# Kernel optimization log

Hardware: AMD Instinct MI355X
Metric: run time of the kernel (lower is better)

Reference implementation:

```python
import jax, jax.numpy as jnp
import numpy as np

B, S, H = 2, 2048, 3072
NH, NKV, HD = 24, 8, 128  # num_heads, num_kv_heads, head_dim


def setup_inputs() -> dict:
    key = jax.random.key(0)
    ks = jax.random.split(key, 5)
    scale = 0.02
    return {
        "hidden_states": jax.random.normal(ks[0], (B, S, H), dtype=jnp.float32),
        "attention_mask": jnp.zeros((B, 1, S, S), dtype=jnp.float32),
        "Wq": jax.random.normal(ks[1], (H, NH * HD), dtype=jnp.float32) * scale,
        "Wk": jax.random.normal(ks[2], (H, NKV * HD), dtype=jnp.float32) * scale,
        "Wv": jax.random.normal(ks[3], (H, NKV * HD), dtype=jnp.float32) * scale,
        "Wo": jax.random.normal(ks[4], (NH * HD, H), dtype=jnp.float32) * scale,
    }


def reference(hidden_states, attention_mask, Wq, Wk, Wv, Wo):
    b, s, _ = hidden_states.shape
    n_rep = NH // NKV
    # projections
    q = (hidden_states @ Wq).reshape(b, s, NH, HD).transpose(0, 2, 1, 3)   # [B,NH,S,D]
    k = (hidden_states @ Wk).reshape(b, s, NKV, HD).transpose(0, 2, 1, 3)  # [B,NKV,S,D]
    v = (hidden_states @ Wv).reshape(b, s, NKV, HD).transpose(0, 2, 1, 3)
    # grouped-query attention: view q as [B, NKV, n_rep, S, D]; avoids materializing repeated KV
    qg = q.reshape(b, NKV, n_rep, s, HD)
    scores = jnp.einsum("bgrqd,bgkd->bgrqk", qg, k) / jnp.sqrt(jnp.float32(HD))
    scores = scores.reshape(b, NH, s, s) + attention_mask
    attn = jax.nn.softmax(scores.astype(jnp.float32), axis=-1).astype(q.dtype)
    out = jnp.einsum("bgrqk,bgkd->bgrqd", attn.reshape(b, NKV, n_rep, s, s), v)
    out = out.reshape(b, NH, s, HD).transpose(0, 2, 1, 3).reshape(b, s, NH * HD)
    return out @ Wo
```

## Files before the change

kernel.cpp:

```cpp
#include <hip/hip_runtime.h>
#include <hip/hip_bf16.h>
#include <stdint.h>

typedef __attribute__((ext_vector_type(8))) short short8;
typedef __attribute__((ext_vector_type(4))) float f32x4;
typedef __attribute__((ext_vector_type(16))) float f32x16;

#define DEVINL static __device__ __forceinline__

DEVINL unsigned short f2bf(float x) {
  union { float f; unsigned int u; } c; c.f = x;
  unsigned int u = c.u;
  u += 0x7fffu + ((u >> 16) & 1u);
  return (unsigned short)(u >> 16);
}

DEVINL float bf2f(unsigned short x) {
  union { unsigned int u; float f; } c; c.u = ((unsigned int)x) << 16;
  return c.f;
}

DEVINL f32x4 mfma16(short8 a, short8 b, f32x4 c) {
  return __builtin_amdgcn_mfma_f32_16x16x32_bf16(a, b, c, 0, 0, 0);
}

DEVINL f32x16 mfma32(short8 a, short8 b, f32x16 c) {
  return __builtin_amdgcn_mfma_f32_32x32x16_bf16(a, b, c, 0, 0, 0);
}

DEVINL unsigned int cvtpk(float lo, float hi_) {
  unsigned int r;
  asm("v_cvt_pk_bf16_f32 %0, %1, %2" : "=v"(r) : "v"(lo), "v"(hi_));
  return r;
}

DEVINL void pl32swap(unsigned int& a, unsigned int& b) {
  asm("v_permlane32_swap_b32 %0, %1" : "+v"(a), "+v"(b));
}

DEVINL void gload16(const void* g, void* l) {
  __builtin_amdgcn_global_load_lds((const __attribute__((address_space(1))) void*)g,
                                   (__attribute__((address_space(3))) void*)l, 16, 0, 0);
}

static constexpr int BB = 2, SS = 2048, HH = 3072;
static constexpr int NH = 24, NKV = 8, HD = 128, NREP = 3;
static constexpr int MM = BB * SS;
static constexpr int KQ = NH * HD;
static constexpr int KKV = NKV * HD;
static constexpr int KV2 = 2 * KKV;

__global__ void k_cvt(const float* __restrict__ in, unsigned short* __restrict__ out,
                      int n, float scale) {
  int i = (blockIdx.x * 256 + threadIdx.x) * 4;
  if (i >= n) return;
  float4 v = *reinterpret_cast<const float4*>(in + i);
  ushort4 o;
  o.x = f2bf(v.x * scale); o.y = f2bf(v.y * scale);
  o.z = f2bf(v.z * scale); o.w = f2bf(v.w * scale);
  *reinterpret_cast<ushort4*>(out + i) = o;
}

__global__ void k_zero(int* p) { *p = 0; }

__global__ void k_cvtm(const float* __restrict__ in, unsigned short* __restrict__ out,
                       int n, float scale, int* __restrict__ flag) {
  int i = (blockIdx.x * 256 + threadIdx.x) * 4;
  if (i >= n) return;
  float4 v = *reinterpret_cast<const float4*>(in + i);
  ushort4 o;
  o.x = f2bf(v.x * scale); o.y = f2bf(v.y * scale);
  o.z = f2bf(v.z * scale); o.w = f2bf(v.w * scale);
  *reinterpret_cast<ushort4*>(out + i) = o;
  bool nz = (v.x != 0.f) || (v.y != 0.f) || (v.z != 0.f) || (v.w != 0.f);
  if (__any(nz) && (threadIdx.x & 63) == 0) atomicOr(flag, 1);
}

__global__ void k_tcvt(const float* __restrict__ in, unsigned short* __restrict__ out,
                       int R, int C, float scale) {
  __shared__ float t[32][33];
  int tx = threadIdx.x & 31, ty = threadIdx.x >> 5;
  int r0 = blockIdx.y * 32, c0 = blockIdx.x * 32;
#pragma unroll
  for (int i = 0; i < 32; i += 8)
    t[ty + i][tx] = in[(long)(r0 + ty + i) * C + c0 + tx];
  __syncthreads();
#pragma unroll
  for (int i = 0; i < 32; i += 8)
    out[(long)(c0 + ty + i) * R + r0 + tx] = f2bf(t[tx][ty + i] * scale);
}

__global__ void k_vt(const unsigned short* __restrict__ KV, unsigned short* __restrict__ VT) {
  __shared__ unsigned short t[32][33];
  int b = blockIdx.z >> 3, kv = blockIdx.z & 7;
  int tx = threadIdx.x & 31, ty = threadIdx.x >> 5;
  int d0 = blockIdx.x * 32, s0 = blockIdx.y * 32;
  const unsigned short* src = KV + ((long)b * SS) * KV2 + KKV + kv * HD;
  unsigned short* dst = VT + (long)(b * NKV + kv) * HD * SS;
#pragma unroll
  for (int i = 0; i < 32; i += 8)
    t[ty + i][tx] = src[(long)(s0 + ty + i) * KV2 + d0 + tx];
  __syncthreads();
#pragma unroll
  for (int i = 0; i < 32; i += 8)
    dst[(long)(d0 + ty + i) * SS + s0 + tx] = t[tx][ty + i];
}

template <typename OutT>
__global__ __launch_bounds__(256, 2) void k_gemm(const unsigned short* __restrict__ A,
                                                 const unsigned short* __restrict__ Bt,
                                                 OutT* __restrict__ C,
                                                 int M, int N, int K) {
  __shared__ alignas(16) unsigned short As[128 * 64];
  __shared__ alignas(16) unsigned short Bs[128 * 64];
  const int tid = threadIdx.x;
  const int wave = tid >> 6, lane = tid & 63;
  const int l15 = lane & 15, g = lane >> 4;
  const int wr = wave >> 1, wc = wave & 1;
  const long m0 = (long)blockIdx.y * 128, n0 = (long)blockIdx.x * 128;

  f32x4 acc[4][4] = {{{0.f,0.f,0.f,0.f}}};

  for (long k0 = 0; k0 < K; k0 += 64) {
#pragma unroll
    for (int j = 0; j < 4; ++j) {
      int idx = j * 256 + wave * 64 + lane;
      int row = idx >> 3, sub = idx & 7;
      int sc_ = (sub ^ (row & 7)) * 8;
      gload16(A  + (m0 + row) * K + k0 + sc_, (char*)As + (j * 4 + wave) * 1024);
      gload16(Bt + (n0 + row) * K + k0 + sc_, (char*)Bs + (j * 4 + wave) * 1024);
    }
    __syncthreads();
#pragma unroll
    for (int ks = 0; ks < 2; ++ks) {
      short8 a[4], b[4];
#pragma unroll
      for (int m = 0; m < 4; ++m) {
        int row = wr * 64 + m * 16 + l15;
        int cb = (ks * 64 + g * 16) ^ ((row & 7) << 4);
        a[m] = *reinterpret_cast<const short8*>((const char*)As + row * 128 + cb);
      }
#pragma unroll
      for (int n = 0; n < 4; ++n) {
        int row = wc * 64 + n * 16 + l15;
        int cb = (ks * 64 + g * 16) ^ ((row & 7) << 4);
        b[n] = *reinterpret_cast<const short8*>((const char*)Bs + row * 128 + cb);
      }
#pragma unroll
      for (int m = 0; m < 4; ++m)
#pragma unroll
        for (int n = 0; n < 4; ++n)
          acc[m][n] = mfma16(a[m], b[n], acc[m][n]);
    }
    __syncthreads();
  }

#pragma unroll
  for (int m = 0; m < 4; ++m)
#pragma unroll
    for (int n = 0; n < 4; ++n)
#pragma unroll
      for (int r = 0; r < 4; ++r) {
        long row = m0 + wr * 64 + m * 16 + g * 4 + r;
        long col = n0 + wc * 64 + n * 16 + l15;
        float v = acc[m][n][r];
        if constexpr (sizeof(OutT) == 2) C[row * N + col] = f2bf(v);
        else                             C[row * N + col] = v;
      }
}

__global__ __launch_bounds__(256, 3) void k_attn(const unsigned short* __restrict__ Q,
                                                 const unsigned short* __restrict__ KV,
                                                 const unsigned short* __restrict__ VT,
                                                 const unsigned short* __restrict__ Mb,
                                                 unsigned short* __restrict__ AO,
                                                 const int* __restrict__ flagp) {
  const int tid = threadIdx.x;
  const int wave = tid >> 6, lane = tid & 63;
  const int l31 = lane & 31, hi = lane >> 5;

  const int bid = blockIdx.x;
  const int id = (bid & 7) * 96 + (bid >> 3);
  const int qt = id & 15;
  const int h  = (id >> 4) % NH;
  const int b  = id / (16 * NH);
  const int kv = h / NREP;
  const int qb = qt * 128 + wave * 32;

  const unsigned short* Qp = Q + ((long)b * SS + qb) * KQ + h * HD;
  const unsigned short* Kp = KV + (long)b * SS * KV2 + kv * HD;
  const unsigned short* Vp = VT + (long)(b * NKV + kv) * HD * SS;
  const unsigned short* Mp = Mb + (long)b * SS * SS + (long)(qb + l31) * SS + hi * 4;

  const int msknz = *flagp;

  __shared__ alignas(16) unsigned short Ks[2][64 * 128];
  __shared__ alignas(16) unsigned short Vs[128 * 64];

  int koff[8], voff[4];
#pragma unroll
  for (int c = 0; c < 8; ++c) {
    int s = c * 2 + hi;
    koff[c] = l31 * 256 + (((s & 8) | ((s ^ (l31 & 7)) & 7)) << 4);
  }
#pragma unroll
  for (int ks = 0; ks < 4; ++ks)
    voff[ks] = l31 * 128 + (((ks * 2 + hi) ^ (l31 & 7)) << 4);

  short8 qf[8];
#pragma unroll
  for (int c = 0; c < 8; ++c)
    qf[c] = *reinterpret_cast<const short8*>(Qp + (long)l31 * KQ + c * 16 + hi * 8);

  f32x16 o[4];
#pragma unroll
  for (int dc = 0; dc < 4; ++dc)
#pragma unroll
    for (int r = 0; r < 16; ++r) o[dc][r] = 0.f;
  float mrun = -3e38f, lrun = 0.f;

  auto stageK = [&](int buf, int kt) {
#pragma unroll
    for (int j = 0; j < 4; ++j) {
      int idx = j * 256 + wave * 64 + lane;
      int row = idx >> 4, s = idx & 15;
      int ss = (s & 8) | ((s ^ row) & 7);
      gload16(Kp + (long)(kt + row) * KV2 + ss * 8,
              (char*)Ks[buf] + (j * 4 + wave) * 1024);
    }
  };
  auto stageV = [&](int kt) {
#pragma unroll
    for (int j = 0; j < 4; ++j) {
      int idx = j * 256 + wave * 64 + lane;
      int row = idx >> 3, s = idx & 7;
      int ss = s ^ (row & 7);
      gload16(Vp + (long)row * SS + kt + ss * 8,
              (char*)Vs + (j * 4 + wave) * 1024);
    }
  };

  stageK(0, 0);
  __syncthreads();

  for (int t = 0; t < SS / 64; ++t) {
    const int kt = t * 64;
    const bool last = (t == SS / 64 - 1);
    stageV(kt);
    if (!last) stageK((t + 1) & 1, kt + 64);

    ushort4 mk[8];
    if (msknz) {
#pragma unroll
      for (int sb = 0; sb < 2; ++sb)
#pragma unroll
        for (int u = 0; u < 4; ++u)
          mk[sb * 4 + u] = *reinterpret_cast<const ushort4*>(Mp + kt + sb * 32 + u * 8);
    }

    f32x16 sc0, sc1;
#pragma unroll
    for (int r = 0; r < 16; ++r) { sc0[r] = 0.f; sc1[r] = 0.f; }
    __builtin_amdgcn_s_setprio(1);
#pragma unroll
    for (int sb = 0; sb < 2; ++sb) {
      const char* kbp = (const char*)Ks[t & 1] + sb * 8192;
#pragma unroll
      for (int c = 0; c < 8; ++c) {
        short8 kf = *reinterpret_cast<const short8*>(kbp + koff[c]);
        if (sb == 0) sc0 = mfma32(kf, qf[c], sc0);
        else         sc1 = mfma32(kf, qf[c], sc1);
      }
    }
    __builtin_amdgcn_s_setprio(0);

    if (msknz) {
#pragma unroll
      for (int sb = 0; sb < 2; ++sb)
#pragma unroll
        for (int u = 0; u < 4; ++u)
#pragma unroll
          for (int e = 0; e < 4; ++e) {
            int r = u * 4 + e;
            if (sb) sc1[r] += bf2f((&mk[sb * 4 + u].x)[e]);
            else    sc0[r] += bf2f((&mk[sb * 4 + u].x)[e]);
          }
    }
    float ta = -3e38f, tb = -3e38f, tc = -3e38f, td = -3e38f;
#pragma unroll
    for (int r = 0; r < 8; ++r) {
      ta = fmaxf(ta, sc0[r]); tb = fmaxf(tb, sc0[r + 8]);
      tc = fmaxf(tc, sc1[r]); td = fmaxf(td, sc1[r + 8]);
    }
    float tm = fmaxf(fmaxf(ta, tb), fmaxf(tc, td));
    tm = fmaxf(tm, __shfl_xor(tm, 32));

    if (!__all(tm <= mrun + 8.f)) {
      float mn = fmaxf(mrun, tm);
      float corr = __builtin_amdgcn_exp2f(mrun - mn);
      mrun = mn;
      lrun *= corr;
#pragma unroll
      for (int r = 0; r < 16; ++r) {
        int qrow = (r & 3) + 8 * (r >> 2) + 4 * hi;
        float cr = __shfl(corr, qrow);
#pragma unroll
        for (int dc = 0; dc < 4; ++dc) o[dc][r] *= cr;
      }
    }

    float s0a = 0.f, s0b = 0.f, s1a = 0.f, s1b = 0.f;
#pragma unroll
    for (int r = 0; r < 8; ++r) {
      sc0[r]     = __builtin_amdgcn_exp2f(sc0[r] - mrun);     s0a += sc0[r];
      sc0[r + 8] = __builtin_amdgcn_exp2f(sc0[r + 8] - mrun); s0b += sc0[r + 8];
      sc1[r]     = __builtin_amdgcn_exp2f(sc1[r] - mrun);     s1a += sc1[r];
      sc1[r + 8] = __builtin_amdgcn_exp2f(sc1[r + 8] - mrun); s1b += sc1[r + 8];
    }
    float ts = (s0a + s0b) + (s1a + s1b);
    ts += __shfl_xor(ts, 32);
    lrun += ts;

    if (!last) asm volatile("s_waitcnt vmcnt(4)" ::: "memory");
    else       asm volatile("s_waitcnt vmcnt(0)" ::: "memory");
    __builtin_amdgcn_s_barrier();

    __builtin_amdgcn_s_setprio(1);
#pragma unroll
    for (int ks = 0; ks < 4; ++ks) {
      const int R = 8 * (ks & 1);
      unsigned int A0, A1, B0, B1;
      if (ks < 2) {
        A0 = cvtpk(sc0[R + 0], sc0[R + 1]); A1 = cvtpk(sc0[R + 2], sc0[R + 3]);
        B0 = cvtpk(sc0[R + 4], sc0[R + 5]); B1 = cvtpk(sc0[R + 6], sc0[R + 7]);
      } else {
        A0 = cvtpk(sc1[R + 0], sc1[R + 1]); A1 = cvtpk(sc1[R + 2], sc1[R + 3]);
        B0 = cvtpk(sc1[R + 4], sc1[R + 5]); B1 = cvtpk(sc1[R + 6], sc1[R + 7]);
      }
      pl32swap(A0, B0);
      pl32swap(A1, B1);
      union { unsigned int w[4]; short8 v; } pa;
      pa.w[0] = A0; pa.w[1] = A1; pa.w[2] = B0; pa.w[3] = B1;
#pragma unroll
      for (int dc = 0; dc < 4; ++dc) {
        short8 vf = *reinterpret_cast<const short8*>((const char*)Vs + dc * 4096 + voff[ks]);
        o[dc] = mfma32(pa.v, vf, o[dc]);
      }
    }
    __builtin_amdgcn_s_setprio(0);

    __syncthreads();
  }

  float inv = 1.f / lrun;
#pragma unroll
  for (int r = 0; r < 16; ++r) {
    int qrow = (r & 3) + 8 * (r >> 2) + 4 * hi;
    float ir = __shfl(inv, qrow);
    long row = qb + qrow;
#pragma unroll
    for (int dc = 0; dc < 4; ++dc)
      AO[((long)b * SS + row) * KQ + h * HD + dc * 32 + l31] = f2bf(o[dc][r] * ir);
  }
}

extern "C" void kernel_launch(void* const* d_in, const int* in_sizes, int n_in,
                              void* d_out, int out_size, void* d_ws, size_t ws_size,
                              hipStream_t stream) {
  const float* hidden = (const float*)d_in[0];
  const float* mask   = (const float*)d_in[1];
  const float* Wq     = (const float*)d_in[2];
  const float* Wk     = (const float*)d_in[3];
  const float* Wv     = (const float*)d_in[4];
  const float* Wo     = (const float*)d_in[5];

  char* ws = (char*)d_ws;
  constexpr long SZ_X   = (long)MM * HH * 2;
  constexpr long SZ_WQT = (long)HH * KQ * 2;
  constexpr long SZ_WKT = (long)HH * KKV * 2;
  constexpr long SZ_QKV = (long)MM * KKV * 2;
  unsigned short* Xb  = (unsigned short*)(ws);
  unsigned short* WqT = (unsigned short*)(ws + SZ_X);
  unsigned short* WkT = (unsigned short*)(ws + SZ_X + SZ_WQT);
  unsigned short* WvT = (unsigned short*)(ws + SZ_X + SZ_WQT + SZ_WKT);
  unsigned short* WoT = (unsigned short*)(ws + SZ_X + SZ_WQT + 2 * SZ_WKT);
  unsigned short* Qb  = (unsigned short*)(ws + SZ_X + 2 * SZ_WQT + 2 * SZ_WKT);
  unsigned short* KVb = (unsigned short*)(ws + 2 * SZ_X + 2 * SZ_WQT + 2 * SZ_WKT);
  unsigned short* VTb = (unsigned short*)(ws + 2 * SZ_X + 2 * SZ_WQT + 2 * SZ_WKT + 2 * SZ_QKV);
  unsigned short* AOb = (unsigned short*)(ws + 2 * SZ_X + 2 * SZ_WQT + 2 * SZ_WKT + 3 * SZ_QKV);
  unsigned short* Mbf = WqT;
  int* flagp = (int*)Xb;

  const float QSCALE = 0.08838834764831845f * 1.4426950408889634f;

  k_cvt<<<(MM * HH) / 1024, 256, 0, stream>>>(hidden, Xb, MM * HH, 1.0f);
  k_tcvt<<<dim3(KQ / 32, HH / 32), 256, 0, stream>>>(Wq, WqT, HH, KQ, QSCALE);
  k_tcvt<<<dim3(KKV / 32, HH / 32), 256, 0, stream>>>(Wk, WkT, HH, KKV, 1.0f);
  k_tcvt<<<dim3(KKV / 32, HH / 32), 256, 0, stream>>>(Wv, WvT, HH, KKV, 1.0f);
  k_tcvt<<<dim3(KQ / 32, HH / 32), 256, 0, stream>>>(Wo, WoT, KQ, HH, 1.0f);

  k_gemm<unsigned short><<<dim3(KQ / 128, MM / 128), 256, 0, stream>>>(Xb, WqT, Qb, MM, KQ, HH);
  k_gemm<unsigned short><<<dim3(KV2 / 128, MM / 128), 256, 0, stream>>>(Xb, WkT, KVb, MM, KV2, HH);

  k_vt<<<dim3(HD / 32, SS / 32, BB * NKV), 256, 0, stream>>>(KVb, VTb);
  k_zero<<<1, 1, 0, stream>>>(flagp);
  k_cvtm<<<(BB * SS * SS) / 1024, 256, 0, stream>>>(mask, Mbf, BB * SS * SS,
                                                    1.4426950408889634f, flagp);

  k_attn<<<16 * NH * BB, 256, 0, stream>>>(Qb, KVb, VTb, Mbf, AOb, flagp);

  k_gemm<float><<<dim3(HH / 128, MM / 128), 256, 0, stream>>>(AOb, WoT, (float*)d_out, MM, HH, HH);
}
```

Measured before the change: 474.7 us.

## Add 256x256 tile GEMM with 512 threads for Q and output projections

```diff
diff --git a/kernel.cpp b/kernel.cpp
--- a/kernel.cpp
+++ b/kernel.cpp
@@ -164,6 +164,126 @@
         long row = m0 + wr * 64 + m * 16 + g * 4 + r;
         long col = n0 + wc * 64 + n * 16 + l15;
         float v = acc[m][n][r];
+        if constexpr (sizeof(OutT) == 2) C[row * N + col] = f2bf(v);
+        else                             C[row * N + col] = v;
+      }
+}
+
+template <typename OutT>
+__global__ __launch_bounds__(512, 2) void k_gemm256(const unsigned short* __restrict__ A,
+                                                    const unsigned short* __restrict__ Bt,
+                                                    OutT* __restrict__ C,
+                                                    int M, int N, int K) {
+  __shared__ alignas(16) unsigned short As[2][256 * 64];
+  __shared__ alignas(16) unsigned short Bs[2][256 * 64];
+  const int tid = threadIdx.x;
+  const int wave = tid >> 6, lane = tid & 63;
+  const int l15 = lane & 15, g = lane >> 4;
+  const int wm = wave >> 2, wn = wave & 3;
+  const long m0 = (long)blockIdx.y * 256, n0 = (long)blockIdx.x * 256;
+  const int nkt = K >> 6;
+
+  f32x4 acc[8][4];
+#pragma unroll
+  for (int mi = 0; mi < 8; ++mi)
+#pragma unroll
+    for (int ni = 0; ni < 4; ++ni)
+      acc[mi][ni] = f32x4{0.f, 0.f, 0.f, 0.f};
+
+  auto stageA = [&](int buf, int kt) {
+#pragma unroll
+    for (int j = 0; j < 4; ++j) {
+      int idx = j * 512 + tid;
+      int row = idx >> 3, s = idx & 7;
+      int ss = s ^ (row & 7);
+      gload16(A + (m0 + row) * K + kt * 64 + ss * 8,
+              (char*)As[buf] + (j * 8 + wave) * 1024);
+    }
+  };
+  auto stageB = [&](int buf, int kt) {
+#pragma unroll
+    for (int j = 0; j < 4; ++j) {
+      int idx = j * 512 + tid;
+      int row = idx >> 3, s = idx & 7;
+      int ss = s ^ (row & 7);
+      gload16(Bt + (n0 + row) * K + kt * 64 + ss * 8,
+              (char*)Bs[buf] + (j * 8 + wave) * 1024);
+    }
+  };
+
+  stageA(0, 0); stageB(0, 0);
+  asm volatile("s_waitcnt vmcnt(0)" ::: "memory");
+  __builtin_amdgcn_s_barrier();
+
+  short8 a[4][2], b[2][2];
+  auto rdA = [&](const char* Ab, int mh) {
+#pragma unroll
+    for (int m = 0; m < 4; ++m) {
+      int R = wm * 128 + mh * 64 + m * 16 + l15;
+#pragma unroll
+      for (int kk = 0; kk < 2; ++kk)
+        a[m][kk] = *reinterpret_cast<const short8*>(
+            Ab + R * 128 + (((kk * 4 + g) ^ (R & 7)) << 4));
+    }
+  };
+  auto rdB = [&](const char* Bb, int nh) {
+#pragma unroll
+    for (int n = 0; n < 2; ++n) {
+      int R = wn * 64 + nh * 32 + n * 16 + l15;
+#pragma unroll
+      for (int kk = 0; kk < 2; ++kk)
+        b[n][kk] = *reinterpret_cast<const short8*>(
+            Bb + R * 128 + (((kk * 4 + g) ^ (R & 7)) << 4));
+    }
+  };
+  auto mm = [&](int mh, int nh) {
+    __builtin_amdgcn_s_setprio(1);
+#pragma unroll
+    for (int m = 0; m < 4; ++m)
+#pragma unroll
+      for (int n = 0; n < 2; ++n)
+#pragma unroll
+        for (int kk = 0; kk < 2; ++kk)
+          acc[mh * 4 + m][nh * 2 + n] =
+              mfma16(a[m][kk], b[n][kk], acc[mh * 4 + m][nh * 2 + n]);
+    __builtin_amdgcn_s_setprio(0);
+  };
+
+  for (int kt = 0; kt < nkt; ++kt) {
+    const int cur = kt & 1;
+    const char* Ab = (const char*)As[cur];
+    const char* Bb = (const char*)Bs[cur];
+    const bool more = (kt + 1 < nkt);
+    if (more) stageA(cur ^ 1, kt + 1);
+    rdA(Ab, 0); rdB(Bb, 0);
+    __builtin_amdgcn_s_barrier();
+    mm(0, 0);
+    __builtin_amdgcn_s_barrier();
+    if (more) stageB(cur ^ 1, kt + 1);
+    rdB(Bb, 1);
+    __builtin_amdgcn_s_barrier();
+    mm(0, 1);
+    __builtin_amdgcn_s_barrier();
+    rdA(Ab, 1); rdB(Bb, 0);
+    __builtin_amdgcn_s_barrier();
+    mm(1, 0);
+    __builtin_amdgcn_s_barrier();
+    rdB(Bb, 1);
+    __builtin_amdgcn_s_barrier();
+    mm(1, 1);
+    asm volatile("s_waitcnt vmcnt(0)" ::: "memory");
+    __builtin_amdgcn_s_barrier();
+  }
+
+#pragma unroll
+  for (int mi = 0; mi < 8; ++mi)
+#pragma unroll
+    for (int ni = 0; ni < 4; ++ni)
+#pragma unroll
+      for (int r = 0; r < 4; ++r) {
+        long row = m0 + wm * 128 + mi * 16 + g * 4 + r;
+        long col = n0 + wn * 64 + ni * 16 + l15;
+        float v = acc[mi][ni][r];
         if constexpr (sizeof(OutT) == 2) C[row * N + col] = f2bf(v);
         else                             C[row * N + col] = v;
       }
@@ -399,7 +519,7 @@
   k_tcvt<<<dim3(KKV / 32, HH / 32), 256, 0, stream>>>(Wv, WvT, HH, KKV, 1.0f);
   k_tcvt<<<dim3(KQ / 32, HH / 32), 256, 0, stream>>>(Wo, WoT, KQ, HH, 1.0f);
 
-  k_gemm<unsigned short><<<dim3(KQ / 128, MM / 128), 256, 0, stream>>>(Xb, WqT, Qb, MM, KQ, HH);
+  k_gemm256<unsigned short><<<dim3(KQ / 256, MM / 256), 512, 0, stream>>>(Xb, WqT, Qb, MM, KQ, HH);
   k_gemm<unsigned short><<<dim3(KV2 / 128, MM / 128), 256, 0, stream>>>(Xb, WkT, KVb, MM, KV2, HH);
 
   k_vt<<<dim3(HD / 32, SS / 32, BB * NKV), 256, 0, stream>>>(KVb, VTb);
@@ -409,5 +529,5 @@
 
   k_attn<<<16 * NH * BB, 256, 0, stream>>>(Qb, KVb, VTb, Mbf, AOb, flagp);
 
-  k_gemm<float><<<dim3(HH / 128, MM / 128), 256, 0, stream>>>(AOb, WoT, (float*)d_out, MM, HH, HH);
-}
+  k_gemm256<float><<<dim3(HH / 256, MM / 256), 512, 0, stream>>>(AOb, WoT, (float*)d_out, MM, HH, HH);
+}
```

After: 555.7 us. +17.1%, slower.

## Read fp32 mask directly in attention and drop bf16 mask conversion pass

Applied to the files above, without the earlier changes.

```diff
diff --git a/kernel.cpp b/kernel.cpp
--- a/kernel.cpp
+++ b/kernel.cpp
@@ -13,11 +13,6 @@
   unsigned int u = c.u;
   u += 0x7fffu + ((u >> 16) & 1u);
   return (unsigned short)(u >> 16);
-}
-
-DEVINL float bf2f(unsigned short x) {
-  union { unsigned int u; float f; } c; c.u = ((unsigned int)x) << 16;
-  return c.f;
 }
 
 DEVINL f32x4 mfma16(short8 a, short8 b, f32x4 c) {
@@ -63,15 +58,10 @@
 
 __global__ void k_zero(int* p) { *p = 0; }
 
-__global__ void k_cvtm(const float* __restrict__ in, unsigned short* __restrict__ out,
-                       int n, float scale, int* __restrict__ flag) {
-  int i = (blockIdx.x * 256 + threadIdx.x) * 4;
-  if (i >= n) return;
-  float4 v = *reinterpret_cast<const float4*>(in + i);
-  ushort4 o;
-  o.x = f2bf(v.x * scale); o.y = f2bf(v.y * scale);
-  o.z = f2bf(v.z * scale); o.w = f2bf(v.w * scale);
-  *reinterpret_cast<ushort4*>(out + i) = o;
+__global__ void k_flag(const float* __restrict__ in, int n4, int* __restrict__ flag) {
+  int i = blockIdx.x * 256 + threadIdx.x;
+  if (i >= n4) return;
+  float4 v = reinterpret_cast<const float4*>(in)[i];
   bool nz = (v.x != 0.f) || (v.y != 0.f) || (v.z != 0.f) || (v.w != 0.f);
   if (__any(nz) && (threadIdx.x & 63) == 0) atomicOr(flag, 1);
 }
@@ -107,7 +97,7 @@
 }
 
 template <typename OutT>
-__global__ __launch_bounds__(256, 2) void k_gemm(const unsigned short* __restrict__ A,
+__global__ __launch_bounds__(256, 3) void k_gemm(const unsigned short* __restrict__ A,
                                                  const unsigned short* __restrict__ Bt,
                                                  OutT* __restrict__ C,
                                                  int M, int N, int K) {
@@ -172,7 +162,7 @@
 __global__ __launch_bounds__(256, 3) void k_attn(const unsigned short* __restrict__ Q,
                                                  const unsigned short* __restrict__ KV,
                                                  const unsigned short* __restrict__ VT,
-                                                 const unsigned short* __restrict__ Mb,
+                                                 const float* __restrict__ Mb,
                                                  unsigned short* __restrict__ AO,
                                                  const int* __restrict__ flagp) {
   const int tid = threadIdx.x;
@@ -190,9 +180,10 @@
   const unsigned short* Qp = Q + ((long)b * SS + qb) * KQ + h * HD;
   const unsigned short* Kp = KV + (long)b * SS * KV2 + kv * HD;
   const unsigned short* Vp = VT + (long)(b * NKV + kv) * HD * SS;
-  const unsigned short* Mp = Mb + (long)b * SS * SS + (long)(qb + l31) * SS + hi * 4;
+  const float* Mp = Mb + ((long)b * SS + qb + l31) * SS + hi * 4;
 
   const int msknz = *flagp;
+  const float LOG2E = 1.4426950408889634f;
 
   __shared__ alignas(16) unsigned short Ks[2][64 * 128];
   __shared__ alignas(16) unsigned short Vs[128 * 64];
@@ -249,13 +240,13 @@
     stageV(kt);
     if (!last) stageK((t + 1) & 1, kt + 64);
 
-    ushort4 mk[8];
+    float4 mk[8];
     if (msknz) {
 #pragma unroll
       for (int sb = 0; sb < 2; ++sb)
 #pragma unroll
         for (int u = 0; u < 4; ++u)
-          mk[sb * 4 + u] = *reinterpret_cast<const ushort4*>(Mp + kt + sb * 32 + u * 8);
+          mk[sb * 4 + u] = *reinterpret_cast<const float4*>(Mp + kt + sb * 32 + u * 8);
     }
 
     f32x16 sc0, sc1;
@@ -282,8 +273,8 @@
 #pragma unroll
           for (int e = 0; e < 4; ++e) {
             int r = u * 4 + e;
-            if (sb) sc1[r] += bf2f((&mk[sb * 4 + u].x)[e]);
-            else    sc0[r] += bf2f((&mk[sb * 4 + u].x)[e]);
+            if (sb) sc1[r] = fmaf((&mk[sb * 4 + u].x)[e], LOG2E, sc1[r]);
+            else    sc0[r] = fmaf((&mk[sb * 4 + u].x)[e], LOG2E, sc0[r]);
           }
     }
     float ta = -3e38f, tb = -3e38f, tc = -3e38f, td = -3e38f;
@@ -388,7 +379,6 @@
   unsigned short* KVb = (unsigned short*)(ws + 2 * SZ_X + 2 * SZ_WQT + 2 * SZ_WKT);
   unsigned short* VTb = (unsigned short*)(ws + 2 * SZ_X + 2 * SZ_WQT + 2 * SZ_WKT + 2 * SZ_QKV);
   unsigned short* AOb = (unsigned short*)(ws + 2 * SZ_X + 2 * SZ_WQT + 2 * SZ_WKT + 3 * SZ_QKV);
-  unsigned short* Mbf = WqT;
   int* flagp = (int*)Xb;
 
   const float QSCALE = 0.08838834764831845f * 1.4426950408889634f;
@@ -404,10 +394,9 @@
 
   k_vt<<<dim3(HD / 32, SS / 32, BB * NKV), 256, 0, stream>>>(KVb, VTb);
   k_zero<<<1, 1, 0, stream>>>(flagp);
-  k_cvtm<<<(BB * SS * SS) / 1024, 256, 0, stream>>>(mask, Mbf, BB * SS * SS,
-                                                    1.4426950408889634f, flagp);
-
-  k_attn<<<16 * NH * BB, 256, 0, stream>>>(Qb, KVb, VTb, Mbf, AOb, flagp);
+  k_flag<<<(BB * SS * SS / 4 + 255) / 256, 256, 0, stream>>>(mask, BB * SS * SS / 4, flagp);
+
+  k_attn<<<16 * NH * BB, 256, 0, stream>>>(Qb, KVb, VTb, mask, AOb, flagp);
 
   k_gemm<float><<<dim3(HH / 128, MM / 128), 256, 0, stream>>>(AOb, WoT, (float*)d_out, MM, HH, HH);
 }
```

Result: faster. 458.2 us (-3.5%).
